# Performance work log

Hardware: AMD Instinct MI355X
Metric: run time of the kernel (lower is better)

## Reference

```python
import jax, jax.numpy as jnp
import numpy as np

B, N, DIM_IN, DIM_OUT, CHEB_K, EMBED_DIM = 64, 2048, 64, 64, 3, 10


def setup_inputs() -> dict:
    key = jax.random.key(0)
    k1, k2, k3, k4 = jax.random.split(key, 4)
    x = jax.random.normal(k1, (B, N, DIM_IN), dtype=jnp.float32)
    node_embeddings = jax.random.normal(k2, (N, EMBED_DIM), dtype=jnp.float32)
    # xavier-normal-like init for the pools
    w_std = (2.0 / (EMBED_DIM * CHEB_K * DIM_IN + DIM_OUT)) ** 0.5
    b_std = (2.0 / (EMBED_DIM + DIM_OUT)) ** 0.5
    weights_pool = jax.random.normal(k3, (EMBED_DIM, CHEB_K, DIM_IN, DIM_OUT), dtype=jnp.float32) * w_std
    bias_pool = jax.random.normal(k4, (EMBED_DIM, DIM_OUT), dtype=jnp.float32) * b_std
    return {"x": x, "node_embeddings": node_embeddings,
            "weights_pool": weights_pool, "bias_pool": bias_pool,
            "cheb_k": CHEB_K}


def reference(x, node_embeddings, weights_pool, bias_pool, cheb_k):
    n = node_embeddings.shape[0]
    # adaptive adjacency: softmax(relu(E E^T)) over neighbors
    supports = jax.nn.softmax(jax.nn.relu(node_embeddings @ node_embeddings.T), axis=1)
    # Chebyshev polynomial supports: T0 = I, T1 = A, Tk = 2 A T_{k-1} - T_{k-2}
    support_set = [jnp.eye(n, dtype=supports.dtype), supports]
    for _ in range(2, cheb_k):
        support_set.append(2.0 * supports @ support_set[-1] - support_set[-2])
    supports_k = jnp.stack(support_set, axis=0)  # [K, N, N]
    # per-node weights and bias synthesized from node embeddings
    weights = jnp.einsum('nd,dkio->nkio', node_embeddings, weights_pool)  # [N, K, I, O]
    bias = node_embeddings @ bias_pool                                    # [N, O]
    # graph convolution
    x_g = jnp.einsum('knm,bmc->bnkc', supports_k, x)                      # [B, N, K, I]
    out = jnp.einsum('bnki,nkio->bno', x_g, weights) + bias               # [B, N, O]
    return out
```

## Files before the change

### kernel.cpp

```cpp
#include <hip/hip_runtime.h>

#define NN 2048
#define BB 64
#define CC 64
#define ED 10
#define KK 3
#define JJ (BB * CC)

typedef unsigned short ushort_t;
typedef __attribute__((ext_vector_type(8))) short short8;
typedef __attribute__((ext_vector_type(4))) float f32x4;

typedef const __attribute__((address_space(1))) unsigned* gptr_t;
typedef __attribute__((address_space(3))) unsigned* lptr_t;
typedef __attribute__((address_space(3))) ushort_t* lsptr_t;
typedef const __attribute__((address_space(3))) short8* ls8_t;

static __device__ __forceinline__ ushort_t f2bf(float f) {
    union { float f; unsigned u; } x{f};
    unsigned r = x.u + 0x7FFF + ((x.u >> 16) & 1);
    return (ushort_t)(r >> 16);
}
static __device__ __forceinline__ float bf2f(ushort_t h) {
    union { unsigned u; float f; } x;
    x.u = ((unsigned)h) << 16;
    return x.f;
}

__global__ __launch_bounds__(256) void prep_kernel(const float* __restrict__ E,
                                                   const float* __restrict__ x,
                                                   const float* __restrict__ Wp,
                                                   ushort_t* __restrict__ Ab,
                                                   ushort_t* __restrict__ xT,
                                                   ushort_t* __restrict__ xN,
                                                   ushort_t* __restrict__ WpT) {
    const int bid = blockIdx.x;
    const int tid = threadIdx.x;

    __shared__ float tb[64][68];
    __shared__ float red[8];

    if (bid < NN) {
        const int n = bid;
        float en[ED];
#pragma unroll
        for (int d = 0; d < ED; ++d) en[d] = E[n * ED + d];

        float sv[NN / 256];
        float lmax = 0.0f;
#pragma unroll
        for (int j = 0; j < NN / 256; ++j) {
            const int m = tid + j * 256;
            const float* Em = E + m * ED;
            float dot = 0.0f;
#pragma unroll
            for (int d = 0; d < ED; ++d) dot += en[d] * Em[d];
            float s = fmaxf(dot, 0.0f);
            sv[j] = s;
            lmax = fmaxf(lmax, s);
        }
#pragma unroll
        for (int off = 32; off > 0; off >>= 1) lmax = fmaxf(lmax, __shfl_down(lmax, off, 64));
        if ((tid & 63) == 0) red[tid >> 6] = lmax;
        __syncthreads();
        const float bmax = fmaxf(fmaxf(red[0], red[1]), fmaxf(red[2], red[3]));

        float lsum = 0.0f;
#pragma unroll
        for (int j = 0; j < NN / 256; ++j) {
            sv[j] = __expf(sv[j] - bmax);
            lsum += sv[j];
        }
#pragma unroll
        for (int off = 32; off > 0; off >>= 1) lsum += __shfl_down(lsum, off, 64);
        if ((tid & 63) == 0) red[4 + (tid >> 6)] = lsum;
        __syncthreads();
        const float inv = 1.0f / (red[4] + red[5] + red[6] + red[7]);

#pragma unroll
        for (int j = 0; j < NN / 256; ++j) {
            Ab[(size_t)n * NN + tid + j * 256] = f2bf(sv[j] * inv);
        }
    } else if (bid < 2 * NN) {
        const int t = bid - NN;
        const int n0 = (t & 31) * 64;
        const int b = t >> 5;

#pragma unroll
        for (int l = 0; l < 4; ++l) {
            const int idx = tid + l * 256;
            const int nn = idx >> 4;
            const int c4 = (idx & 15) << 2;
            const float4 v = *(const float4*)(x + ((size_t)b * NN + n0 + nn) * CC + c4);
            tb[c4 + 0][nn] = v.x;
            tb[c4 + 1][nn] = v.y;
            tb[c4 + 2][nn] = v.z;
            tb[c4 + 3][nn] = v.w;
        }
        __syncthreads();

#pragma unroll
        for (int l = 0; l < 2; ++l) {
            const int idx = tid + l * 256;
            const int c = idx >> 3;
            const int ch = (idx & 7) << 3;
            ushort_t pack[8];
#pragma unroll
            for (int e = 0; e < 8; ++e) pack[e] = f2bf(tb[c][ch + e]);
            *(float4*)(xT + (size_t)(b * 64 + c) * NN + n0 + ch) = *(float4*)pack;
        }
#pragma unroll
        for (int l = 0; l < 2; ++l) {
            const int idx = tid + l * 256;
            const int nn = idx >> 3;
            const int cg = (idx & 7) << 3;
            ushort_t pack[8];
#pragma unroll
            for (int e = 0; e < 8; ++e) pack[e] = f2bf(tb[cg + e][nn]);
            *(float4*)(xN + (size_t)(n0 + nn) * JJ + b * 64 + cg) = *(float4*)pack;
        }
    } else {
        const int dk = bid - 2 * NN;
        const float* src = Wp + (size_t)dk * CC * CC;

#pragma unroll
        for (int l = 0; l < 4; ++l) {
            const int idx = tid + l * 256;
            const int i = idx >> 4;
            const int o4 = (idx & 15) << 2;
            const float4 v = *(const float4*)(src + i * CC + o4);
            tb[o4 + 0][i] = v.x;
            tb[o4 + 1][i] = v.y;
            tb[o4 + 2][i] = v.z;
            tb[o4 + 3][i] = v.w;
        }
        __syncthreads();

#pragma unroll
        for (int l = 0; l < 2; ++l) {
            const int idx = tid + l * 256;
            const int o = idx >> 3;
            const int ic = (idx & 7) << 3;
            ushort_t pack[8];
#pragma unroll
            for (int e = 0; e < 8; ++e) pack[e] = f2bf(tb[o][ic + e]);
            *(float4*)(WpT + (size_t)dk * CC * CC + o * CC + ic) = *(float4*)pack;
        }
    }
}

#define STAGE_A(bp, kt) do {                                                                \
    __builtin_amdgcn_global_load_lds(                                                       \
        (gptr_t)(srcA + (size_t)(kt) * 64),                                                 \
        (lptr_t)&(bp)[dstoff], 16, 0, 0);                                                   \
    __builtin_amdgcn_global_load_lds(                                                       \
        (gptr_t)(srcA + (size_t)64 * NN + (size_t)(kt) * 64),                               \
        (lptr_t)&(bp)[4096 + dstoff], 16, 0, 0);                                            \
} while (0)

#define STAGE_B(bp, h, kt) do {                                                             \
    __builtin_amdgcn_global_load_lds(                                                       \
        (gptr_t)(srcB + (size_t)((h) * 2) * 64 * NN + (size_t)(kt) * 64),                   \
        (lptr_t)&(bp)[8192 + (h) * 8192 + dstoff], 16, 0, 0);                               \
    __builtin_amdgcn_global_load_lds(                                                       \
        (gptr_t)(srcB + (size_t)((h) * 2 + 1) * 64 * NN + (size_t)(kt) * 64),               \
        (lptr_t)&(bp)[8192 + (h) * 8192 + 4096 + dstoff], 16, 0, 0);                        \
} while (0)

#define LDA_ALL(bp) do {                                                                    \
    _Pragma("unroll") for (int mi_ = 0; mi_ < 4; ++mi_)                                     \
    _Pragma("unroll") for (int ks_ = 0; ks_ < 2; ++ks_)                                     \
        a[mi_][ks_] = *(ls8_t)&(bp)[(aRG + mi_) * 1024 + ks_ * 512 + rdofs];                \
} while (0)

#define LDB_H(bp, h) do {                                                                   \
    _Pragma("unroll") for (int nn_ = 0; nn_ < 2; ++nn_)                                     \
    _Pragma("unroll") for (int ks_ = 0; ks_ < 2; ++ks_)                                     \
        b[(h) * 2 + nn_][ks_] =                                                             \
            *(ls8_t)&(bp)[8192 + (bRG + (h) * 2 + nn_) * 1024 + ks_ * 512 + rdofs];         \
} while (0)

#define MFMA_C(c) do {                                                                      \
    __builtin_amdgcn_s_setprio(1);                                                          \
    _Pragma("unroll") for (int mi_ = 0; mi_ < 4; ++mi_)                                     \
    _Pragma("unroll") for (int nn_ = 0; nn_ < 2; ++nn_) {                                   \
        acc[mi_][(c) * 2 + nn_] = __builtin_amdgcn_mfma_f32_16x16x32_bf16(                  \
            a[mi_][0], b[(c) * 2 + nn_][0], acc[mi_][(c) * 2 + nn_], 0, 0, 0);              \
        acc[mi_][(c) * 2 + nn_] = __builtin_amdgcn_mfma_f32_16x16x32_bf16(                  \
            a[mi_][1], b[(c) * 2 + nn_][1], acc[mi_][(c) * 2 + nn_], 0, 0, 0);              \
    }                                                                                       \
    __builtin_amdgcn_s_setprio(0);                                                          \
} while (0)

template <int MODE>
__global__ __launch_bounds__(512, 2) void gemm_roll(const ushort_t* __restrict__ A,
                                                    const ushort_t* __restrict__ Bt,
                                                    const ushort_t* __restrict__ Zn,
                                                    ushort_t* __restrict__ Ct,
                                                    ushort_t* __restrict__ Cn) {
    int bid = blockIdx.x;
    bid = (bid & 7) * 32 + (bid >> 3);
    const int bx = bid & 15;
    const int by = bid >> 4;
    const int j0 = bx * 256;
    const int m0 = by * 128;

    const int tid = threadIdx.x;
    const int w = tid >> 6;
    const int lane = tid & 63;
    const int l16 = lane & 15;
    const int quad = lane >> 4;
    const int wm = (w >> 2) * 64;
    const int wn = (w & 3) * 64;
    const int aRG = (w >> 2) * 4;
    const int bRG = (w & 3) * 4;
    const int rdofs = l16 * 32 + ((quad * 8) ^ ((l16 & 8) * 2));

    const int r16s = lane >> 2;
    const int cx = (lane & 3) ^ ((r16s >> 3) << 1);
    const int rowbase = (w >> 1) * 16 + r16s;
    const int kofs = (w & 1) * 32 + cx * 8;
    const ushort_t* srcA = A + (size_t)(m0 + rowbase) * NN + kofs;
    const ushort_t* srcB = Bt + (size_t)(j0 + rowbase) * NN + kofs;
    const int dstoff = tid * 8;

    __shared__ ushort_t lds[3][24576];

    lsptr_t p0 = (lsptr_t)&lds[0][0];
    lsptr_t p1 = (lsptr_t)&lds[1][0];
    lsptr_t p2 = (lsptr_t)&lds[2][0];

    f32x4 acc[4][4];
#pragma unroll
    for (int mi = 0; mi < 4; ++mi)
#pragma unroll
        for (int ni = 0; ni < 4; ++ni) acc[mi][ni] = (f32x4){0.f, 0.f, 0.f, 0.f};

    short8 a[4][2], b[4][2];

    STAGE_A(p0, 0); STAGE_B(p0, 0, 0); STAGE_B(p0, 1, 0);
    STAGE_A(p1, 1); STAGE_B(p1, 0, 1); STAGE_B(p1, 1, 1);

#pragma unroll 1
    for (int t = 0; t < 32; ++t) {
        if (t) MFMA_C(1);
        if (t < 31) { asm volatile("s_waitcnt vmcnt(6)" ::: "memory"); }
        else        { asm volatile("s_waitcnt vmcnt(0)" ::: "memory"); }
        __builtin_amdgcn_sched_barrier(0);
        __builtin_amdgcn_s_barrier();

        LDA_ALL(p0); LDB_H(p0, 0);
        const bool stg = (t < 30);
        if (stg) { STAGE_A(p2, t + 2); STAGE_B(p2, 0, t + 2); }
        asm volatile("s_waitcnt lgkmcnt(0)" ::: "memory");
        __builtin_amdgcn_sched_barrier(0);
        MFMA_C(0);
        LDB_H(p0, 1);
        if (stg) STAGE_B(p2, 1, t + 2);
        __builtin_amdgcn_sched_barrier(0);

        lsptr_t tp = p0; p0 = p1; p1 = p2; p2 = tp;
    }
    MFMA_C(1);

#pragma unroll
    for (int mi = 0; mi < 4; ++mi) {
#pragma unroll
        for (int ji = 0; ji < 4; ++ji) {
            const int j = j0 + wn + ji * 16 + l16;
            const int mb = m0 + wm + mi * 16 + quad * 4;
            if (MODE == 0) {
                ushort_t o[4];
#pragma unroll
                for (int r = 0; r < 4; ++r) o[r] = f2bf(acc[mi][ji][r]);
                *(unsigned long long*)(Ct + (size_t)j * NN + mb) = *(unsigned long long*)o;
#pragma unroll
                for (int r = 0; r < 4; ++r) Cn[(size_t)(mb + r) * JJ + j] = o[r];
            } else {
#pragma unroll
                for (int r = 0; r < 4; ++r) {
                    const float z = bf2f(Zn[(size_t)(mb + r) * JJ + j]);
                    Cn[(size_t)(mb + r) * JJ + j] = f2bf(2.0f * acc[mi][ji][r] - z);
                }
            }
        }
    }
}

#undef STAGE_A
#undef STAGE_B
#undef LDA_ALL
#undef LDB_H
#undef MFMA_C

#define XLD 200
__global__ __launch_bounds__(256) void out_kernel(const float* __restrict__ E,
                                                  const ushort_t* __restrict__ WpT,
                                                  const float* __restrict__ bp,
                                                  const ushort_t* __restrict__ xN,
                                                  const ushort_t* __restrict__ y1N,
                                                  const ushort_t* __restrict__ y2N,
                                                  float* __restrict__ out) {
    const int n = blockIdx.x;
    const int tid = threadIdx.x;

    __shared__ ushort_t xg[BB * XLD];
    __shared__ ushort_t Wt[CC * XLD];
    __shared__ float en_s[ED];
    __shared__ float bias_s[CC];

    if (tid < ED) en_s[tid] = E[n * ED + tid];
    __syncthreads();

    float en[ED];
#pragma unroll
    for (int d = 0; d < ED; ++d) en[d] = en_s[d];

    if (tid < CC) {
        float bsum = 0.0f;
#pragma unroll
        for (int d = 0; d < ED; ++d) bsum += en[d] * bp[d * CC + tid];
        bias_s[tid] = bsum;
    }

#pragma unroll
    for (int k = 0; k < KK; ++k) {
        const ushort_t* src = (k == 0) ? xN : (k == 1) ? y1N : y2N;
        const float4* srow = (const float4*)(src + (size_t)n * JJ);
        for (int idx = tid; idx < JJ / 8; idx += 256) {
            *(float4*)&xg[(idx >> 3) * XLD + k * 64 + ((idx & 7) << 3)] = srow[idx];
        }
    }

    for (int t = tid; t < CC * 24; t += 256) {
        const int o = t / 24;
        const int kc = t % 24;
        const int k = kc >> 3;
        const int ic = (kc & 7) << 3;
        float s[8];
#pragma unroll
        for (int e = 0; e < 8; ++e) s[e] = 0.0f;
#pragma unroll
        for (int d = 0; d < ED; ++d) {
            const float4 wv4 = *(const float4*)(WpT + ((size_t)(d * KK + k) * CC + o) * CC + ic);
            const ushort_t* wp = (const ushort_t*)&wv4;
#pragma unroll
            for (int e = 0; e < 8; ++e) s[e] += en[d] * bf2f(wp[e]);
        }
        ushort_t pack[8];
#pragma unroll
        for (int e = 0; e < 8; ++e) pack[e] = f2bf(s[e]);
        *(float4*)&Wt[o * XLD + k * 64 + ic] = *(float4*)pack;
    }
    __syncthreads();

    const int lane = tid & 63;
    const int l16 = lane & 15;
    const int quad = lane >> 4;
    const int bm = (tid >> 6) * 16;

    f32x4 acc[4];
#pragma unroll
    for (int ji = 0; ji < 4; ++ji) acc[ji] = (f32x4){0.f, 0.f, 0.f, 0.f};

#pragma unroll
    for (int kc = 0; kc < 6; ++kc) {
        const short8 av = *(const short8*)&xg[(bm + l16) * XLD + kc * 32 + quad * 8];
#pragma unroll
        for (int ji = 0; ji < 4; ++ji) {
            const short8 bv = *(const short8*)&Wt[(ji * 16 + l16) * XLD + kc * 32 + quad * 8];
            acc[ji] = __builtin_amdgcn_mfma_f32_16x16x32_bf16(av, bv, acc[ji], 0, 0, 0);
        }
    }

#pragma unroll
    for (int ji = 0; ji < 4; ++ji) {
        const int o = ji * 16 + l16;
        const float bo = bias_s[o];
#pragma unroll
        for (int r = 0; r < 4; ++r) {
            const int b = bm + quad * 4 + r;
            out[((size_t)b * NN + n) * CC + o] = acc[ji][r] + bo;
        }
    }
}
#undef XLD

extern "C" void kernel_launch(void* const* d_in, const int* in_sizes, int n_in,
                              void* d_out, int out_size, void* d_ws, size_t ws_size,
                              hipStream_t stream) {
    const float* x  = (const float*)d_in[0];
    const float* E  = (const float*)d_in[1];
    const float* Wp = (const float*)d_in[2];
    const float* bp = (const float*)d_in[3];

    ushort_t* Ab  = (ushort_t*)d_ws;
    ushort_t* xT  = Ab + (size_t)NN * NN;
    ushort_t* xN  = xT + (size_t)JJ * NN;
    ushort_t* y1T = xN + (size_t)NN * JJ;
    ushort_t* y1N = y1T + (size_t)JJ * NN;
    ushort_t* y2N = y1N + (size_t)NN * JJ;
    ushort_t* WpT = y2N + (size_t)NN * JJ;
    float* out = (float*)d_out;

    prep_kernel<<<2 * NN + ED * KK, 256, 0, stream>>>(E, x, Wp, Ab, xT, xN, WpT);
    gemm_roll<0><<<256, 512, 0, stream>>>(Ab, xT, nullptr, y1T, y1N);
    gemm_roll<1><<<256, 512, 0, stream>>>(Ab, y1T, xN, nullptr, y2N);
    out_kernel<<<NN, 256, 0, stream>>>(E, WpT, bp, xN, y1N, y2N, out);
}
```

Measured before the change: 204.4 us.

## Halve GEMM block threads, give each wave a 64x128 tile

The rolled GEMM now runs 256 threads (4 waves) per block instead of 512. Each wave computes a 64x128 output tile with 8 B fragments and 32 accumulators, and each thread issues 12 global-to-LDS loads per stage. The aim is more MFMA reuse per LDS read and less per-block overhead, paid for with roughly doubled accumulator registers and fewer waves to hide latency. The softmax prep loop also reads embeddings as float2 pairs.

Result: slower. 212.6 us (+4.0%).

```diff
diff --git a/kernel.cpp b/kernel.cpp
--- a/kernel.cpp
+++ b/kernel.cpp
@@ -51,10 +51,13 @@
 #pragma unroll
         for (int j = 0; j < NN / 256; ++j) {
             const int m = tid + j * 256;
-            const float* Em = E + m * ED;
+            const float2* Em2 = (const float2*)(E + m * ED);
             float dot = 0.0f;
 #pragma unroll
-            for (int d = 0; d < ED; ++d) dot += en[d] * Em[d];
+            for (int d2 = 0; d2 < ED / 2; ++d2) {
+                const float2 v = Em2[d2];
+                dot += en[2 * d2] * v.x + en[2 * d2 + 1] * v.y;
+            }
             float s = fmaxf(dot, 0.0f);
             sv[j] = s;
             lmax = fmaxf(lmax, s);
@@ -149,22 +152,15 @@
     }
 }
 
-#define STAGE_A(bp, kt) do {                                                                \
-    __builtin_amdgcn_global_load_lds(                                                       \
-        (gptr_t)(srcA + (size_t)(kt) * 64),                                                 \
-        (lptr_t)&(bp)[dstoff], 16, 0, 0);                                                   \
-    __builtin_amdgcn_global_load_lds(                                                       \
-        (gptr_t)(srcA + (size_t)64 * NN + (size_t)(kt) * 64),                               \
-        (lptr_t)&(bp)[4096 + dstoff], 16, 0, 0);                                            \
-} while (0)
-
-#define STAGE_B(bp, h, kt) do {                                                             \
-    __builtin_amdgcn_global_load_lds(                                                       \
-        (gptr_t)(srcB + (size_t)((h) * 2) * 64 * NN + (size_t)(kt) * 64),                   \
-        (lptr_t)&(bp)[8192 + (h) * 8192 + dstoff], 16, 0, 0);                               \
-    __builtin_amdgcn_global_load_lds(                                                       \
-        (gptr_t)(srcB + (size_t)((h) * 2 + 1) * 64 * NN + (size_t)(kt) * 64),               \
-        (lptr_t)&(bp)[8192 + (h) * 8192 + 4096 + dstoff], 16, 0, 0);                        \
+#define STAGE_AB(bp, kt) do {                                                               \
+    _Pragma("unroll") for (int i_ = 0; i_ < 4; ++i_)                                        \
+        __builtin_amdgcn_global_load_lds(                                                   \
+            (gptr_t)(srcA + (size_t)(kt) * 64 + (size_t)i_ * 32 * NN),                      \
+            (lptr_t)&(bp)[dstoff + i_ * 2048], 16, 0, 0);                                   \
+    _Pragma("unroll") for (int i_ = 0; i_ < 8; ++i_)                                        \
+        __builtin_amdgcn_global_load_lds(                                                   \
+            (gptr_t)(srcB + (size_t)(kt) * 64 + (size_t)i_ * 32 * NN),                      \
+            (lptr_t)&(bp)[8192 + dstoff + i_ * 2048], 16, 0, 0);                            \
 } while (0)
 
 #define LDA_ALL(bp) do {                                                                    \
@@ -173,27 +169,32 @@
         a[mi_][ks_] = *(ls8_t)&(bp)[(aRG + mi_) * 1024 + ks_ * 512 + rdofs];                \
 } while (0)
 
-#define LDB_H(bp, h) do {                                                                   \
-    _Pragma("unroll") for (int nn_ = 0; nn_ < 2; ++nn_)                                     \
+#define LDB_LO(bp) do {                                                                     \
+    _Pragma("unroll") for (int ni_ = 0; ni_ < 4; ++ni_)                                     \
     _Pragma("unroll") for (int ks_ = 0; ks_ < 2; ++ks_)                                     \
-        b[(h) * 2 + nn_][ks_] =                                                             \
-            *(ls8_t)&(bp)[8192 + (bRG + (h) * 2 + nn_) * 1024 + ks_ * 512 + rdofs];         \
+        b[ni_][ks_] = *(ls8_t)&(bp)[8192 + (bRG + ni_) * 1024 + ks_ * 512 + rdofs];         \
+} while (0)
+
+#define LDB_HI(bp) do {                                                                     \
+    _Pragma("unroll") for (int ni_ = 4; ni_ < 8; ++ni_)                                     \
+    _Pragma("unroll") for (int ks_ = 0; ks_ < 2; ++ks_)                                     \
+        b[ni_][ks_] = *(ls8_t)&(bp)[8192 + (bRG + ni_) * 1024 + ks_ * 512 + rdofs];         \
 } while (0)
 
 #define MFMA_C(c) do {                                                                      \
     __builtin_amdgcn_s_setprio(1);                                                          \
     _Pragma("unroll") for (int mi_ = 0; mi_ < 4; ++mi_)                                     \
-    _Pragma("unroll") for (int nn_ = 0; nn_ < 2; ++nn_) {                                   \
-        acc[mi_][(c) * 2 + nn_] = __builtin_amdgcn_mfma_f32_16x16x32_bf16(                  \
-            a[mi_][0], b[(c) * 2 + nn_][0], acc[mi_][(c) * 2 + nn_], 0, 0, 0);              \
-        acc[mi_][(c) * 2 + nn_] = __builtin_amdgcn_mfma_f32_16x16x32_bf16(                  \
-            a[mi_][1], b[(c) * 2 + nn_][1], acc[mi_][(c) * 2 + nn_], 0, 0, 0);              \
+    _Pragma("unroll") for (int nn_ = 0; nn_ < 4; ++nn_) {                                   \
+        acc[mi_][(c) * 4 + nn_] = __builtin_amdgcn_mfma_f32_16x16x32_bf16(                  \
+            a[mi_][0], b[(c) * 4 + nn_][0], acc[mi_][(c) * 4 + nn_], 0, 0, 0);              \
+        acc[mi_][(c) * 4 + nn_] = __builtin_amdgcn_mfma_f32_16x16x32_bf16(                  \
+            a[mi_][1], b[(c) * 4 + nn_][1], acc[mi_][(c) * 4 + nn_], 0, 0, 0);              \
     }                                                                                       \
     __builtin_amdgcn_s_setprio(0);                                                          \
 } while (0)
 
 template <int MODE>
-__global__ __launch_bounds__(512, 2) void gemm_roll(const ushort_t* __restrict__ A,
+__global__ __launch_bounds__(256, 1) void gemm_roll(const ushort_t* __restrict__ A,
                                                     const ushort_t* __restrict__ Bt,
                                                     const ushort_t* __restrict__ Zn,
                                                     ushort_t* __restrict__ Ct,
@@ -210,18 +211,19 @@
     const int lane = tid & 63;
     const int l16 = lane & 15;
     const int quad = lane >> 4;
-    const int wm = (w >> 2) * 64;
-    const int wn = (w & 3) * 64;
-    const int aRG = (w >> 2) * 4;
-    const int bRG = (w & 3) * 4;
+    const int wm = (w >> 1) * 64;
+    const int wn = (w & 1) * 128;
+    const int aRG = (w >> 1) * 4;
+    const int bRG = (w & 1) * 8;
     const int rdofs = l16 * 32 + ((quad * 8) ^ ((l16 & 8) * 2));
 
-    const int r16s = lane >> 2;
-    const int cx = (lane & 3) ^ ((r16s >> 3) << 1);
-    const int rowbase = (w >> 1) * 16 + r16s;
-    const int kofs = (w & 1) * 32 + cx * 8;
-    const ushort_t* srcA = A + (size_t)(m0 + rowbase) * NN + kofs;
-    const ushort_t* srcB = Bt + (size_t)(j0 + rowbase) * NN + kofs;
+    const int r16s = (tid >> 2) & 15;
+    const int q4 = tid & 3;
+    const int cx = q4 ^ ((r16s >> 3) << 1);
+    const int rowg0 = (tid >> 7) * 16 + r16s;
+    const int kofs = ((tid >> 6) & 1) * 32 + cx * 8;
+    const ushort_t* srcA = A + (size_t)(m0 + rowg0) * NN + kofs;
+    const ushort_t* srcB = Bt + (size_t)(j0 + rowg0) * NN + kofs;
     const int dstoff = tid * 8;
 
     __shared__ ushort_t lds[3][24576];
@@ -230,33 +232,31 @@
     lsptr_t p1 = (lsptr_t)&lds[1][0];
     lsptr_t p2 = (lsptr_t)&lds[2][0];
 
-    f32x4 acc[4][4];
+    f32x4 acc[4][8];
 #pragma unroll
     for (int mi = 0; mi < 4; ++mi)
 #pragma unroll
-        for (int ni = 0; ni < 4; ++ni) acc[mi][ni] = (f32x4){0.f, 0.f, 0.f, 0.f};
-
-    short8 a[4][2], b[4][2];
-
-    STAGE_A(p0, 0); STAGE_B(p0, 0, 0); STAGE_B(p0, 1, 0);
-    STAGE_A(p1, 1); STAGE_B(p1, 0, 1); STAGE_B(p1, 1, 1);
+        for (int ni = 0; ni < 8; ++ni) acc[mi][ni] = (f32x4){0.f, 0.f, 0.f, 0.f};
+
+    short8 a[4][2], b[8][2];
+
+    STAGE_AB(p0, 0);
+    STAGE_AB(p1, 1);
 
 #pragma unroll 1
     for (int t = 0; t < 32; ++t) {
         if (t) MFMA_C(1);
-        if (t < 31) { asm volatile("s_waitcnt vmcnt(6)" ::: "memory"); }
+        if (t < 31) { asm volatile("s_waitcnt vmcnt(12)" ::: "memory"); }
         else        { asm volatile("s_waitcnt vmcnt(0)" ::: "memory"); }
         __builtin_amdgcn_sched_barrier(0);
         __builtin_amdgcn_s_barrier();
 
-        LDA_ALL(p0); LDB_H(p0, 0);
-        const bool stg = (t < 30);
-        if (stg) { STAGE_A(p2, t + 2); STAGE_B(p2, 0, t + 2); }
+        LDA_ALL(p0); LDB_LO(p0);
+        if (t < 30) STAGE_AB(p2, t + 2);
         asm volatile("s_waitcnt lgkmcnt(0)" ::: "memory");
         __builtin_amdgcn_sched_barrier(0);
         MFMA_C(0);
-        LDB_H(p0, 1);
-        if (stg) STAGE_B(p2, 1, t + 2);
+        LDB_HI(p0);
         __builtin_amdgcn_sched_barrier(0);
 
         lsptr_t tp = p0; p0 = p1; p1 = p2; p2 = tp;
@@ -266,7 +266,7 @@
 #pragma unroll
     for (int mi = 0; mi < 4; ++mi) {
 #pragma unroll
-        for (int ji = 0; ji < 4; ++ji) {
+        for (int ji = 0; ji < 8; ++ji) {
             const int j = j0 + wn + ji * 16 + l16;
             const int mb = m0 + wm + mi * 16 + quad * 4;
             if (MODE == 0) {
@@ -287,10 +287,10 @@
     }
 }
 
-#undef STAGE_A
-#undef STAGE_B
+#undef STAGE_AB
 #undef LDA_ALL
-#undef LDB_H
+#undef LDB_LO
+#undef LDB_HI
 #undef MFMA_C
 
 #define XLD 200
@@ -404,7 +404,7 @@
     float* out = (float*)d_out;
 
     prep_kernel<<<2 * NN + ED * KK, 256, 0, stream>>>(E, x, Wp, Ab, xT, xN, WpT);
-    gemm_roll<0><<<256, 512, 0, stream>>>(Ab, xT, nullptr, y1T, y1N);
-    gemm_roll<1><<<256, 512, 0, stream>>>(Ab, y1T, xN, nullptr, y2N);
+    gemm_roll<0><<<256, 256, 0, stream>>>(Ab, xT, nullptr, y1T, y1N);
+    gemm_roll<1><<<256, 256, 0, stream>>>(Ab, y1T, xN, nullptr, y2N);
     out_kernel<<<NN, 256, 0, stream>>>(E, WpT, bp, xN, y1N, y2N, out);
 }
```

## Restructure GEMM main loop with double-buffered register fragments and unified staging

Applied to the files above, without the earlier changes.

The bf16 MFMA GEMM loop is rewritten to handle two K-tiles per iteration. The A and B fragments for the next tile are read from LDS into a second register set while MFMAs run on the current set, and all A and B global-to-LDS copies for a tile are issued together. The goal is to hide LDS read latency behind MFMA work. In exchange it uses more registers for fragments, and each barrier now waits on vmcnt(0), which shortens how far ahead global loads run. The prep kernel also reads node embeddings as float2 in the softmax dot product.

Result: no change. 208.3 us (+1.9%).

```diff
diff --git a/kernel.cpp b/kernel.cpp
--- a/kernel.cpp
+++ b/kernel.cpp
@@ -51,10 +51,13 @@
 #pragma unroll
         for (int j = 0; j < NN / 256; ++j) {
             const int m = tid + j * 256;
-            const float* Em = E + m * ED;
+            const float2* Em2 = (const float2*)(E + m * ED);
             float dot = 0.0f;
 #pragma unroll
-            for (int d = 0; d < ED; ++d) dot += en[d] * Em[d];
+            for (int d2 = 0; d2 < ED / 2; ++d2) {
+                const float2 v = Em2[d2];
+                dot += en[2 * d2] * v.x + en[2 * d2 + 1] * v.y;
+            }
             float s = fmaxf(dot, 0.0f);
             sv[j] = s;
             lmax = fmaxf(lmax, s);
@@ -149,51 +152,48 @@
     }
 }
 
-#define STAGE_A(bp, kt) do {                                                                \
+#define STAGE_ALL(bp, kt) do {                                                              \
     __builtin_amdgcn_global_load_lds(                                                       \
         (gptr_t)(srcA + (size_t)(kt) * 64),                                                 \
         (lptr_t)&(bp)[dstoff], 16, 0, 0);                                                   \
     __builtin_amdgcn_global_load_lds(                                                       \
         (gptr_t)(srcA + (size_t)64 * NN + (size_t)(kt) * 64),                               \
         (lptr_t)&(bp)[4096 + dstoff], 16, 0, 0);                                            \
+    _Pragma("unroll") for (int u_ = 0; u_ < 4; ++u_)                                        \
+        __builtin_amdgcn_global_load_lds(                                                   \
+            (gptr_t)(srcB + (size_t)(u_ * 64) * NN + (size_t)(kt) * 64),                    \
+            (lptr_t)&(bp)[8192 + u_ * 4096 + dstoff], 16, 0, 0);                            \
 } while (0)
 
-#define STAGE_B(bp, h, kt) do {                                                             \
-    __builtin_amdgcn_global_load_lds(                                                       \
-        (gptr_t)(srcB + (size_t)((h) * 2) * 64 * NN + (size_t)(kt) * 64),                   \
-        (lptr_t)&(bp)[8192 + (h) * 8192 + dstoff], 16, 0, 0);                               \
-    __builtin_amdgcn_global_load_lds(                                                       \
-        (gptr_t)(srcB + (size_t)((h) * 2 + 1) * 64 * NN + (size_t)(kt) * 64),               \
-        (lptr_t)&(bp)[8192 + (h) * 8192 + 4096 + dstoff], 16, 0, 0);                        \
-} while (0)
-
-#define LDA_ALL(bp) do {                                                                    \
+#define READ_FRAGS(aa, bb, bp) do {                                                         \
     _Pragma("unroll") for (int mi_ = 0; mi_ < 4; ++mi_)                                     \
     _Pragma("unroll") for (int ks_ = 0; ks_ < 2; ++ks_)                                     \
-        a[mi_][ks_] = *(ls8_t)&(bp)[(aRG + mi_) * 1024 + ks_ * 512 + rdofs];                \
+        aa[mi_][ks_] = *(ls8_t)&(bp)[(aRG + mi_) * 1024 + ks_ * 512 + rdofs];               \
+    _Pragma("unroll") for (int ni_ = 0; ni_ < 4; ++ni_)                                     \
+    _Pragma("unroll") for (int ks_ = 0; ks_ < 2; ++ks_)                                     \
+        bb[ni_][ks_] = *(ls8_t)&(bp)[8192 + (bRG + ni_) * 1024 + ks_ * 512 + rdofs];        \
 } while (0)
 
-#define LDB_H(bp, h) do {                                                                   \
-    _Pragma("unroll") for (int nn_ = 0; nn_ < 2; ++nn_)                                     \
-    _Pragma("unroll") for (int ks_ = 0; ks_ < 2; ++ks_)                                     \
-        b[(h) * 2 + nn_][ks_] =                                                             \
-            *(ls8_t)&(bp)[8192 + (bRG + (h) * 2 + nn_) * 1024 + ks_ * 512 + rdofs];         \
-} while (0)
-
-#define MFMA_C(c) do {                                                                      \
+#define MFMA_SET(aa, bb) do {                                                               \
     __builtin_amdgcn_s_setprio(1);                                                          \
     _Pragma("unroll") for (int mi_ = 0; mi_ < 4; ++mi_)                                     \
-    _Pragma("unroll") for (int nn_ = 0; nn_ < 2; ++nn_) {                                   \
-        acc[mi_][(c) * 2 + nn_] = __builtin_amdgcn_mfma_f32_16x16x32_bf16(                  \
-            a[mi_][0], b[(c) * 2 + nn_][0], acc[mi_][(c) * 2 + nn_], 0, 0, 0);              \
-        acc[mi_][(c) * 2 + nn_] = __builtin_amdgcn_mfma_f32_16x16x32_bf16(                  \
-            a[mi_][1], b[(c) * 2 + nn_][1], acc[mi_][(c) * 2 + nn_], 0, 0, 0);              \
+    _Pragma("unroll") for (int ni_ = 0; ni_ < 4; ++ni_) {                                   \
+        acc[mi_][ni_] = __builtin_amdgcn_mfma_f32_16x16x32_bf16(                            \
+            aa[mi_][0], bb[ni_][0], acc[mi_][ni_], 0, 0, 0);                                \
+        acc[mi_][ni_] = __builtin_amdgcn_mfma_f32_16x16x32_bf16(                            \
+            aa[mi_][1], bb[ni_][1], acc[mi_][ni_], 0, 0, 0);                                \
     }                                                                                       \
     __builtin_amdgcn_s_setprio(0);                                                          \
 } while (0)
 
+#define TILE_TOP do {                                                                       \
+    asm volatile("s_waitcnt vmcnt(0)" ::: "memory");                                        \
+    __builtin_amdgcn_s_barrier();                                                           \
+    __builtin_amdgcn_sched_barrier(0);                                                      \
+} while (0)
+
 template <int MODE>
-__global__ __launch_bounds__(512, 2) void gemm_roll(const ushort_t* __restrict__ A,
+__global__ __launch_bounds__(512, 2) void gemm_pipe(const ushort_t* __restrict__ A,
                                                     const ushort_t* __restrict__ Bt,
                                                     const ushort_t* __restrict__ Zn,
                                                     ushort_t* __restrict__ Ct,
@@ -236,32 +236,31 @@
 #pragma unroll
         for (int ni = 0; ni < 4; ++ni) acc[mi][ni] = (f32x4){0.f, 0.f, 0.f, 0.f};
 
-    short8 a[4][2], b[4][2];
-
-    STAGE_A(p0, 0); STAGE_B(p0, 0, 0); STAGE_B(p0, 1, 0);
-    STAGE_A(p1, 1); STAGE_B(p1, 0, 1); STAGE_B(p1, 1, 1);
+    short8 a0[4][2], b0[4][2], a1[4][2], b1[4][2];
+
+    STAGE_ALL(p0, 0);
+    STAGE_ALL(p1, 1);
+    asm volatile("s_waitcnt vmcnt(6)" ::: "memory");
+    __builtin_amdgcn_s_barrier();
+    __builtin_amdgcn_sched_barrier(0);
+    READ_FRAGS(a0, b0, p0);
 
 #pragma unroll 1
-    for (int t = 0; t < 32; ++t) {
-        if (t) MFMA_C(1);
-        if (t < 31) { asm volatile("s_waitcnt vmcnt(6)" ::: "memory"); }
-        else        { asm volatile("s_waitcnt vmcnt(0)" ::: "memory"); }
-        __builtin_amdgcn_sched_barrier(0);
-        __builtin_amdgcn_s_barrier();
-
-        LDA_ALL(p0); LDB_H(p0, 0);
-        const bool stg = (t < 30);
-        if (stg) { STAGE_A(p2, t + 2); STAGE_B(p2, 0, t + 2); }
-        asm volatile("s_waitcnt lgkmcnt(0)" ::: "memory");
-        __builtin_amdgcn_sched_barrier(0);
-        MFMA_C(0);
-        LDB_H(p0, 1);
-        if (stg) STAGE_B(p2, 1, t + 2);
-        __builtin_amdgcn_sched_barrier(0);
-
-        lsptr_t tp = p0; p0 = p1; p1 = p2; p2 = tp;
-    }
-    MFMA_C(1);
+    for (int i = 0; i < 16; ++i) {
+        const bool stg = (i < 15);
+        TILE_TOP;
+        if (stg) STAGE_ALL(p2, 2 * i + 2);
+        READ_FRAGS(a1, b1, p1);
+        MFMA_SET(a0, b0);
+        TILE_TOP;
+        if (stg) {
+            STAGE_ALL(p0, 2 * i + 3);
+            READ_FRAGS(a0, b0, p2);
+        }
+        MFMA_SET(a1, b1);
+        lsptr_t q0 = p0, q1 = p1, q2 = p2;
+        p0 = q2; p1 = q0; p2 = q1;
+    }
 
 #pragma unroll
     for (int mi = 0; mi < 4; ++mi) {
@@ -287,11 +286,10 @@
     }
 }
 
-#undef STAGE_A
-#undef STAGE_B
-#undef LDA_ALL
-#undef LDB_H
-#undef MFMA_C
+#undef STAGE_ALL
+#undef READ_FRAGS
+#undef MFMA_SET
+#undef TILE_TOP
 
 #define XLD 200
 __global__ __launch_bounds__(256) void out_kernel(const float* __restrict__ E,
@@ -404,7 +402,7 @@
     float* out = (float*)d_out;
 
     prep_kernel<<<2 * NN + ED * KK, 256, 0, stream>>>(E, x, Wp, Ab, xT, xN, WpT);
-    gemm_roll<0><<<256, 512, 0, stream>>>(Ab, xT, nullptr, y1T, y1N);
-    gemm_roll<1><<<256, 512, 0, stream>>>(Ab, y1T, xN, nullptr, y2N);
+    gemm_pipe<0><<<256, 512, 0, stream>>>(Ab, xT, nullptr, y1T, y1N);
+    gemm_pipe<1><<<256, 512, 0, stream>>>(Ab, y1T, xN, nullptr, y2N);
     out_kernel<<<NN, 256, 0, stream>>>(E, WpT, bp, xN, y1N, y2N, out);
 }
```

## Move Chebyshev recurrence subtraction from GEMM epilogue into output kernel

Applied to the files above, without the earlier changes.

The second GEMM now stores the raw A·y1 product, dropping its strided read of x. The 2·A·y1 − x combination is done in out_kernel while it loads x, which it already reads, so one full pass over x is no longer needed. That raw product reuses the xT workspace buffer, and out_kernel now handles two nodes per 512-thread block. The prep kernel also reads embedding rows as float2 pairs. Risks: the product is rounded to bf16 before the subtraction, adding a rounding step, and out_kernel's doubled LDS footprint may lower occupancy.

New measurement: 212.9 us. 4.2% more time.

```diff
diff --git a/kernel.cpp b/kernel.cpp
--- a/kernel.cpp
+++ b/kernel.cpp
@@ -51,10 +51,13 @@
 #pragma unroll
         for (int j = 0; j < NN / 256; ++j) {
             const int m = tid + j * 256;
-            const float* Em = E + m * ED;
+            const float2* Em2 = (const float2*)(E + m * ED);
             float dot = 0.0f;
 #pragma unroll
-            for (int d = 0; d < ED; ++d) dot += en[d] * Em[d];
+            for (int d2 = 0; d2 < ED / 2; ++d2) {
+                const float2 v = Em2[d2];
+                dot += en[2 * d2] * v.x + en[2 * d2 + 1] * v.y;
+            }
             float s = fmaxf(dot, 0.0f);
             sv[j] = s;
             lmax = fmaxf(lmax, s);
@@ -195,7 +198,6 @@
 template <int MODE>
 __global__ __launch_bounds__(512, 2) void gemm_roll(const ushort_t* __restrict__ A,
                                                     const ushort_t* __restrict__ Bt,
-                                                    const ushort_t* __restrict__ Zn,
                                                     ushort_t* __restrict__ Ct,
                                                     ushort_t* __restrict__ Cn) {
     int bid = blockIdx.x;
@@ -269,20 +271,14 @@
         for (int ji = 0; ji < 4; ++ji) {
             const int j = j0 + wn + ji * 16 + l16;
             const int mb = m0 + wm + mi * 16 + quad * 4;
+            ushort_t o[4];
+#pragma unroll
+            for (int r = 0; r < 4; ++r) o[r] = f2bf(acc[mi][ji][r]);
             if (MODE == 0) {
-                ushort_t o[4];
-#pragma unroll
-                for (int r = 0; r < 4; ++r) o[r] = f2bf(acc[mi][ji][r]);
                 *(unsigned long long*)(Ct + (size_t)j * NN + mb) = *(unsigned long long*)o;
-#pragma unroll
-                for (int r = 0; r < 4; ++r) Cn[(size_t)(mb + r) * JJ + j] = o[r];
-            } else {
-#pragma unroll
-                for (int r = 0; r < 4; ++r) {
-                    const float z = bf2f(Zn[(size_t)(mb + r) * JJ + j]);
-                    Cn[(size_t)(mb + r) * JJ + j] = f2bf(2.0f * acc[mi][ji][r] - z);
-                }
             }
+#pragma unroll
+            for (int r = 0; r < 4; ++r) Cn[(size_t)(mb + r) * JJ + j] = o[r];
         }
     }
 }
@@ -294,45 +290,60 @@
 #undef MFMA_C
 
 #define XLD 200
-__global__ __launch_bounds__(256) void out_kernel(const float* __restrict__ E,
+__global__ __launch_bounds__(512) void out_kernel(const float* __restrict__ E,
                                                   const ushort_t* __restrict__ WpT,
                                                   const float* __restrict__ bp,
                                                   const ushort_t* __restrict__ xN,
                                                   const ushort_t* __restrict__ y1N,
-                                                  const ushort_t* __restrict__ y2N,
+                                                  const ushort_t* __restrict__ y2r,
                                                   float* __restrict__ out) {
-    const int n = blockIdx.x;
     const int tid = threadIdx.x;
-
-    __shared__ ushort_t xg[BB * XLD];
-    __shared__ ushort_t Wt[CC * XLD];
-    __shared__ float en_s[ED];
-    __shared__ float bias_s[CC];
-
-    if (tid < ED) en_s[tid] = E[n * ED + tid];
+    const int half = tid >> 8;
+    const int t8 = tid & 255;
+    const int n = blockIdx.x * 2 + half;
+
+    __shared__ ushort_t xg[2][BB * XLD];
+    __shared__ ushort_t Wt[2][CC * XLD];
+    __shared__ float en_s[2][ED];
+    __shared__ float bias_s[2][CC];
+
+    if (t8 < ED) en_s[half][t8] = E[n * ED + t8];
     __syncthreads();
 
     float en[ED];
 #pragma unroll
-    for (int d = 0; d < ED; ++d) en[d] = en_s[d];
-
-    if (tid < CC) {
+    for (int d = 0; d < ED; ++d) en[d] = en_s[half][d];
+
+    if (t8 < CC) {
         float bsum = 0.0f;
 #pragma unroll
-        for (int d = 0; d < ED; ++d) bsum += en[d] * bp[d * CC + tid];
-        bias_s[tid] = bsum;
-    }
-
-#pragma unroll
-    for (int k = 0; k < KK; ++k) {
-        const ushort_t* src = (k == 0) ? xN : (k == 1) ? y1N : y2N;
-        const float4* srow = (const float4*)(src + (size_t)n * JJ);
-        for (int idx = tid; idx < JJ / 8; idx += 256) {
-            *(float4*)&xg[(idx >> 3) * XLD + k * 64 + ((idx & 7) << 3)] = srow[idx];
-        }
-    }
-
-    for (int t = tid; t < CC * 24; t += 256) {
+        for (int d = 0; d < ED; ++d) bsum += en[d] * bp[d * CC + t8];
+        bias_s[half][t8] = bsum;
+    }
+
+    {
+        const float4* sx = (const float4*)(xN + (size_t)n * JJ);
+        const float4* s1 = (const float4*)(y1N + (size_t)n * JJ);
+        const float4* s2 = (const float4*)(y2r + (size_t)n * JJ);
+        for (int idx = t8; idx < JJ / 8; idx += 256) {
+            const float4 xv = sx[idx];
+            const float4 v1 = s1[idx];
+            const float4 v2 = s2[idx];
+            const int row = idx >> 3;
+            const int col = (idx & 7) << 3;
+            *(float4*)&xg[half][row * XLD + col] = xv;
+            *(float4*)&xg[half][row * XLD + 64 + col] = v1;
+            ushort_t pk[8];
+            const ushort_t* px = (const ushort_t*)&xv;
+            const ushort_t* p2 = (const ushort_t*)&v2;
+#pragma unroll
+            for (int e = 0; e < 8; ++e)
+                pk[e] = f2bf(2.0f * bf2f(p2[e]) - bf2f(px[e]));
+            *(float4*)&xg[half][row * XLD + 128 + col] = *(float4*)pk;
+        }
+    }
+
+    for (int t = t8; t < CC * 24; t += 256) {
         const int o = t / 24;
         const int kc = t % 24;
         const int k = kc >> 3;
@@ -350,14 +361,14 @@
         ushort_t pack[8];
 #pragma unroll
         for (int e = 0; e < 8; ++e) pack[e] = f2bf(s[e]);
-        *(float4*)&Wt[o * XLD + k * 64 + ic] = *(float4*)pack;
+        *(float4*)&Wt[half][o * XLD + k * 64 + ic] = *(float4*)pack;
     }
     __syncthreads();
 
-    const int lane = tid & 63;
+    const int lane = t8 & 63;
     const int l16 = lane & 15;
     const int quad = lane >> 4;
-    const int bm = (tid >> 6) * 16;
+    const int bm = (t8 >> 6) * 16;
 
     f32x4 acc[4];
 #pragma unroll
@@ -365,10 +376,10 @@
 
 #pragma unroll
     for (int kc = 0; kc < 6; ++kc) {
-        const short8 av = *(const short8*)&xg[(bm + l16) * XLD + kc * 32 + quad * 8];
+        const short8 av = *(const short8*)&xg[half][(bm + l16) * XLD + kc * 32 + quad * 8];
 #pragma unroll
         for (int ji = 0; ji < 4; ++ji) {
-            const short8 bv = *(const short8*)&Wt[(ji * 16 + l16) * XLD + kc * 32 + quad * 8];
+            const short8 bv = *(const short8*)&Wt[half][(ji * 16 + l16) * XLD + kc * 32 + quad * 8];
             acc[ji] = __builtin_amdgcn_mfma_f32_16x16x32_bf16(av, bv, acc[ji], 0, 0, 0);
         }
     }
@@ -376,7 +387,7 @@
 #pragma unroll
     for (int ji = 0; ji < 4; ++ji) {
         const int o = ji * 16 + l16;
-        const float bo = bias_s[o];
+        const float bo = bias_s[half][o];
 #pragma unroll
         for (int r = 0; r < 4; ++r) {
             const int b = bm + quad * 4 + r;
@@ -399,12 +410,12 @@
     ushort_t* xN  = xT + (size_t)JJ * NN;
     ushort_t* y1T = xN + (size_t)NN * JJ;
     ushort_t* y1N = y1T + (size_t)JJ * NN;
-    ushort_t* y2N = y1N + (size_t)NN * JJ;
-    ushort_t* WpT = y2N + (size_t)NN * JJ;
+    ushort_t* WpT = y1N + (size_t)NN * JJ;
+    ushort_t* y2r = xT;
     float* out = (float*)d_out;
 
     prep_kernel<<<2 * NN + ED * KK, 256, 0, stream>>>(E, x, Wp, Ab, xT, xN, WpT);
-    gemm_roll<0><<<256, 512, 0, stream>>>(Ab, xT, nullptr, y1T, y1N);
-    gemm_roll<1><<<256, 512, 0, stream>>>(Ab, y1T, xN, nullptr, y2N);
-    out_kernel<<<NN, 256, 0, stream>>>(E, WpT, bp, xN, y1N, y2N, out);
-}
+    gemm_roll<0><<<256, 512, 0, stream>>>(Ab, xT, y1T, y1N);
+    gemm_roll<1><<<256, 512, 0, stream>>>(Ab, y1T, nullptr, y2r);
+    out_kernel<<<NN / 2, 512, 0, stream>>>(E, WpT, bp, xN, y1N, y2r, out);
+}
```
